# Kernel tuning notes

Measured on AMD Instinct MI355X. Metric: run time of the kernel, lower is better.

The kernel has to match this reference:

```python
import jax, jax.numpy as jnp
import numpy as np

B, L, D, U = 4, 1024, 256, 32

def setup_inputs() -> dict:
    key = jax.random.key(0)
    k1, k2, k3, k4 = jax.random.split(key, 4)
    return {
        "inputs": jax.random.normal(k1, (B, L, D), dtype=jnp.float32),
        "Wt": jax.random.normal(k2, (D, U), dtype=jnp.float32) * (1.0 / np.sqrt(D)),
        "Wx": jax.random.normal(k3, (D, U), dtype=jnp.float32) * (1.0 / np.sqrt(D)),
        "bh": jnp.zeros((U,), dtype=jnp.float32),
        "Wa": jax.random.normal(k4, (U, 1), dtype=jnp.float32) * (1.0 / np.sqrt(U)),
        "ba": jnp.zeros((1,), dtype=jnp.float32),
    }


def reference(inputs, Wt, Wx, bh, Wa, ba):
    # inputs: [B, L, D]
    q = jnp.einsum('bld,du->blu', inputs, Wt)  # [B, L, U]
    k = jnp.einsum('bld,du->blu', inputs, Wx)  # [B, L, U]
    # additive (Bahdanau) pairwise score: h is [B, L, L, U]
    h = jnp.tanh(q[:, :, None, :] + k[:, None, :, :] + bh)
    e = jnp.einsum('biju,u->bij', h, Wa[:, 0]) + ba[0]  # [B, L, L]
    a = jax.nn.softmax(e, axis=-1)  # stable softmax == exp(e-max)/sum
    v = jnp.einsum('bij,bjd->bid', a, inputs)  # weighted sum, [B, L, D]
    return v
```

## Files before the change

kernel.cpp:

```cpp
#include <hip/hip_runtime.h>
#include <hip/hip_bf16.h>
#include <math.h>

#define B_ 4
#define L_ 1024
#define D_ 256
#define U_ 32

#define SC2 2.8853900817779268f

#if __has_builtin(__builtin_amdgcn_exp2f)
#define EXP2(x) __builtin_amdgcn_exp2f(x)
#else
#define EXP2(x) exp2f(x)
#endif
#if __has_builtin(__builtin_amdgcn_rcpf)
#define RCP(x) __builtin_amdgcn_rcpf(x)
#else
#define RCP(x) (1.0f / (x))
#endif

typedef __attribute__((ext_vector_type(8))) short bf16x8;
typedef __attribute__((ext_vector_type(4))) float f32x4;
typedef unsigned long long u64;

__device__ __forceinline__ ushort f2bf(float f) {
  uint b = __float_as_uint(f);
  return (ushort)((b + 0x7fffu + ((b >> 16) & 1u)) >> 16);
}
__device__ __forceinline__ float bf2f(ushort u) {
  return __uint_as_float(((uint)u) << 16);
}
__device__ __forceinline__ uint packhl(float v) {
  ushort h = f2bf(v);
  ushort l = f2bf(v - bf2f(h));
  return (((uint)h) << 16) | (uint)l;
}
__device__ __forceinline__ u64 hi64(uint4 p) {
  return ((u64)(p.x >> 16)) | ((u64)(p.y >> 16) << 16) |
         ((u64)(p.z >> 16) << 32) | ((u64)(p.w >> 16) << 48);
}
__device__ __forceinline__ u64 lo64(uint4 p) {
  return ((u64)(p.x & 0xffffu)) | ((u64)(p.y & 0xffffu) << 16) |
         ((u64)(p.z & 0xffffu) << 32) | ((u64)(p.w & 0xffffu) << 48);
}

__global__ __launch_bounds__(256) void k_proj(
    const float* __restrict__ x, const float* __restrict__ Wt,
    const float* __restrict__ Wx, const float* __restrict__ bh,
    float* __restrict__ q2, float* __restrict__ k2, uint* __restrict__ xpk) {
  const int row = blockIdx.x;
  const int t = threadIdx.x;
  __shared__ float xr[D_];
  __shared__ float part[256];
  const float xv = x[(size_t)row * D_ + t];
  xr[t] = xv;
  {
    const int b = row >> 10;
    const int l = row & (L_ - 1);
    xpk[((size_t)b * D_ + t) * L_ + l] = packhl(xv);
  }
  __syncthreads();
  const int out = t & 63;
  const int u = out & 31;
  const int sel = out >> 5;
  const int p = t >> 6;
  const float* W = sel ? Wx : Wt;
  float s = 0.f;
  #pragma unroll
  for (int d = 0; d < 64; ++d) {
    const int dd = p * 64 + d;
    s = fmaf(xr[dd], W[dd * U_ + u], s);
  }
  part[t] = s;
  __syncthreads();
  if (t < 64) {
    const float v = part[t] + part[t + 64] + part[t + 128] + part[t + 192];
    if (sel == 0)
      q2[(size_t)row * U_ + u] = SC2 * (v + bh[u]);
    else
      k2[(size_t)row * U_ + u] = SC2 * v;
  }
}

__global__ __launch_bounds__(512) void k_scores(
    const float* __restrict__ q2, const float* __restrict__ k2,
    const float* __restrict__ Wa, uint* __restrict__ apk) {
  const int blk = blockIdx.x;
  const int b = blk >> 7;
  const int i0 = (blk & 127) * 8;
  const int t = threadIdx.x;
  __shared__ float e_lds[8][L_];

  const float* kb = k2 + (size_t)b * L_ * U_;
  float kr0[32], kr1[32];
  #pragma unroll
  for (int c = 0; c < 8; ++c) {
    const float4 v0 = *(const float4*)&kb[(size_t)t * U_ + 4 * c];
    const float4 v1 = *(const float4*)&kb[(size_t)(t + 512) * U_ + 4 * c];
    kr0[4 * c] = v0.x; kr0[4 * c + 1] = v0.y; kr0[4 * c + 2] = v0.z; kr0[4 * c + 3] = v0.w;
    kr1[4 * c] = v1.x; kr1[4 * c + 1] = v1.y; kr1[4 * c + 2] = v1.z; kr1[4 * c + 3] = v1.w;
  }

  float wa[32];
  float sumwa = 0.f;
  #pragma unroll
  for (int u = 0; u < 32; ++u) { wa[u] = Wa[u]; sumwa += wa[u]; }

  const float* qb = q2 + ((size_t)(b * L_ + i0)) * U_;
  #pragma unroll
  for (int i = 0; i < 8; ++i) {
    float qv[32];
    #pragma unroll
    for (int u = 0; u < 32; ++u) qv[u] = qb[i * U_ + u];
    float a00 = 0.f, a01 = 0.f, a10 = 0.f, a11 = 0.f;
    #pragma unroll
    for (int u = 0; u < 32; u += 2) {
      {
        const float y0 = qv[u] + kr0[u];
        const float r0 = RCP(EXP2(y0) + 1.f);
        a00 = fmaf(wa[u], r0, a00);
        const float y1 = qv[u] + kr1[u];
        const float r1 = RCP(EXP2(y1) + 1.f);
        a10 = fmaf(wa[u], r1, a10);
      }
      {
        const float y0 = qv[u + 1] + kr0[u + 1];
        const float r0 = RCP(EXP2(y0) + 1.f);
        a01 = fmaf(wa[u + 1], r0, a01);
        const float y1 = qv[u + 1] + kr1[u + 1];
        const float r1 = RCP(EXP2(y1) + 1.f);
        a11 = fmaf(wa[u + 1], r1, a11);
      }
    }
    e_lds[i][t]       = sumwa - 2.f * (a00 + a01);
    e_lds[i][t + 512] = sumwa - 2.f * (a10 + a11);
  }
  __syncthreads();

  const int w = t >> 6;
  const int lane = t & 63;
  float ev[16];
  float m = -1e30f;
  #pragma unroll
  for (int mm = 0; mm < 16; ++mm) {
    ev[mm] = e_lds[w][lane + 64 * mm];
    m = fmaxf(m, ev[mm]);
  }
  #pragma unroll
  for (int off = 32; off >= 1; off >>= 1) m = fmaxf(m, __shfl_xor(m, off, 64));
  float s = 0.f;
  #pragma unroll
  for (int mm = 0; mm < 16; ++mm) { ev[mm] = __expf(ev[mm] - m); s += ev[mm]; }
  #pragma unroll
  for (int off = 32; off >= 1; off >>= 1) s += __shfl_xor(s, off, 64);
  const float rinv = 1.0f / s;
  uint* arow = apk + ((size_t)(b * L_ + i0 + w)) * L_;
  #pragma unroll
  for (int mm = 0; mm < 16; ++mm) arow[lane + 64 * mm] = packhl(ev[mm] * rinv);
}

#define MFMA16(A, Bf, C) __builtin_amdgcn_mfma_f32_16x16x32_bf16(A, Bf, C, 0, 0, 0)

__global__ __launch_bounds__(256) void k_wsum(
    const uint* __restrict__ apk, const uint* __restrict__ xpk,
    float* __restrict__ out) {
  const int d0 = blockIdx.x * 64;
  const int i0 = blockIdx.y * 64;
  const int b  = blockIdx.z;
  const int t  = threadIdx.x;
  const int lane = t & 63;
  const int w  = t >> 6;
  const int wr = w >> 1;
  const int wc = w & 1;

  __shared__ f32x4 ldsv[4 * 64 * 8];
  char* const base = (char*)ldsv;

  const int r = t >> 2;
  const int q = t & 3;
  const uint* asrc = apk + ((size_t)(b * L_ + i0 + r)) * L_ + q * 16;
  const uint* xsrc = xpk + ((size_t)(b * D_ + d0 + r)) * L_ + q * 16;

  f32x4 acc00 = {0.f, 0.f, 0.f, 0.f}, acc01 = {0.f, 0.f, 0.f, 0.f};
  f32x4 acc10 = {0.f, 0.f, 0.f, 0.f}, acc11 = {0.f, 0.f, 0.f, 0.f};

  uint4 ra[4], rx[4];
  #pragma unroll
  for (int c = 0; c < 4; ++c) {
    ra[c] = *(const uint4*)(asrc + 4 * c);
    rx[c] = *(const uint4*)(xsrc + 4 * c);
  }

  for (int step = 0; step < 16; ++step) {
    __syncthreads();
    #pragma unroll
    for (int c = 0; c < 4; ++c) {
      const int jj = q * 16 + 4 * c;
      const int u = jj >> 3;
      const int half = (jj >> 2) & 1;
      const int off = r * 128 + ((u ^ (r & 7)) << 4) + half * 8;
      *(u64*)(base + off)          = hi64(ra[c]);
      *(u64*)(base + off + 8192)   = lo64(ra[c]);
      *(u64*)(base + off + 16384)  = hi64(rx[c]);
      *(u64*)(base + off + 24576)  = lo64(rx[c]);
    }
    if (step < 15) {
      #pragma unroll
      for (int c = 0; c < 4; ++c) {
        ra[c] = *(const uint4*)(asrc + (step + 1) * 64 + 4 * c);
        rx[c] = *(const uint4*)(xsrc + (step + 1) * 64 + 4 * c);
      }
    }
    __syncthreads();

    #pragma unroll
    for (int ks = 0; ks < 2; ++ks) {
      const int ub = ks * 4 + (lane >> 4);
      auto frag = [&](int plane, int rbase) -> bf16x8 {
        const int rr = rbase + (lane & 15);
        const int off = plane * 8192 + rr * 128 + ((ub ^ (rr & 7)) << 4);
        return *(const bf16x8*)(base + off);
      };
      const bf16x8 ah0 = frag(0, wr * 32), ah1 = frag(0, wr * 32 + 16);
      const bf16x8 al0 = frag(1, wr * 32), al1 = frag(1, wr * 32 + 16);
      const bf16x8 xh0 = frag(2, wc * 32), xh1 = frag(2, wc * 32 + 16);
      const bf16x8 xl0 = frag(3, wc * 32), xl1 = frag(3, wc * 32 + 16);
      acc00 = MFMA16(ah0, xh0, acc00); acc00 = MFMA16(al0, xh0, acc00); acc00 = MFMA16(ah0, xl0, acc00);
      acc01 = MFMA16(ah0, xh1, acc01); acc01 = MFMA16(al0, xh1, acc01); acc01 = MFMA16(ah0, xl1, acc01);
      acc10 = MFMA16(ah1, xh0, acc10); acc10 = MFMA16(al1, xh0, acc10); acc10 = MFMA16(ah1, xl0, acc10);
      acc11 = MFMA16(ah1, xh1, acc11); acc11 = MFMA16(al1, xh1, acc11); acc11 = MFMA16(ah1, xl1, acc11);
    }
  }

  const int crow = (lane >> 4) * 4;
  const int ccol = lane & 15;
  #pragma unroll
  for (int m2 = 0; m2 < 2; ++m2) {
    #pragma unroll
    for (int n2 = 0; n2 < 2; ++n2) {
      const f32x4 acc = m2 == 0 ? (n2 == 0 ? acc00 : acc01)
                                : (n2 == 0 ? acc10 : acc11);
      const int col = d0 + wc * 32 + n2 * 16 + ccol;
      #pragma unroll
      for (int jj = 0; jj < 4; ++jj) {
        const int rowi = i0 + wr * 32 + m2 * 16 + crow + jj;
        out[((size_t)(b * L_ + rowi)) * D_ + col] = acc[jj];
      }
    }
  }
}

extern "C" void kernel_launch(void* const* d_in, const int* in_sizes, int n_in,
                              void* d_out, int out_size, void* d_ws, size_t ws_size,
                              hipStream_t stream) {
  const float* x  = (const float*)d_in[0];
  const float* Wt = (const float*)d_in[1];
  const float* Wx = (const float*)d_in[2];
  const float* bh = (const float*)d_in[3];
  const float* Wa = (const float*)d_in[4];
  float* out = (float*)d_out;
  float* ws = (float*)d_ws;
  float* q2 = ws;
  float* k2 = ws + (size_t)B_ * L_ * U_;
  uint* apk = (uint*)(ws + (size_t)2 * B_ * L_ * U_);
  uint* xpk = apk + (size_t)B_ * L_ * L_;
  if (ws_size < (size_t)22020096) return;

  k_proj<<<B_ * L_, 256, 0, stream>>>(x, Wt, Wx, bh, q2, k2, xpk);
  k_scores<<<B_ * (L_ / 8), 512, 0, stream>>>(q2, k2, Wa, apk);
  dim3 g3(D_ / 64, L_ / 64, B_);
  k_wsum<<<g3, 256, 0, stream>>>(apk, xpk, out);
}
```

Baseline: 153.2 us.

## Split-K the weighted-sum GEMM, batch projection rows, and vectorize LDS stores

The weighted-sum kernel is split four ways along the key dimension, so the grid grows from 256 to 1024 blocks. Partial sums go to a workspace buffer and a new reduce kernel adds them. The projection kernel now handles 16 rows per block with float4 weight loads and writes coalesced uint4 packed-x stores instead of scattered scalar ones, and the wsum LDS staging uses 128-bit stores. The split adds a 16 MB partial-sum write and read plus an extra kernel launch.

Result: faster. 134.1 us, median of 2 (-12.5%).

```diff
diff --git a/kernel.cpp b/kernel.cpp
--- a/kernel.cpp
+++ b/kernel.cpp
@@ -6,6 +6,7 @@
 #define L_ 1024
 #define D_ 256
 #define U_ 32
+#define KSPLIT 4
 
 #define SC2 2.8853900817779268f
 
@@ -44,42 +45,75 @@
   return ((u64)(p.x & 0xffffu)) | ((u64)(p.y & 0xffffu) << 16) |
          ((u64)(p.z & 0xffffu) << 32) | ((u64)(p.w & 0xffffu) << 48);
 }
+__device__ __forceinline__ uint4 mk128(u64 lo, u64 hi) {
+  uint4 r;
+  r.x = (uint)lo; r.y = (uint)(lo >> 32);
+  r.z = (uint)hi; r.w = (uint)(hi >> 32);
+  return r;
+}
 
 __global__ __launch_bounds__(256) void k_proj(
     const float* __restrict__ x, const float* __restrict__ Wt,
     const float* __restrict__ Wx, const float* __restrict__ bh,
     float* __restrict__ q2, float* __restrict__ k2, uint* __restrict__ xpk) {
-  const int row = blockIdx.x;
+  const int blk = blockIdx.x;
+  const int b = blk >> 6;
+  const int l0 = (blk & 63) * 16;
   const int t = threadIdx.x;
-  __shared__ float xr[D_];
-  __shared__ float part[256];
-  const float xv = x[(size_t)row * D_ + t];
-  xr[t] = xv;
+  __shared__ float xr[16][D_];
+
+  const float* xbase = x + ((size_t)(b * L_ + l0)) * D_;
   {
-    const int b = row >> 10;
-    const int l = row & (L_ - 1);
-    xpk[((size_t)b * D_ + t) * L_ + l] = packhl(xv);
+    const int r = t >> 4;
+    const int c0 = (t & 15) * 16;
+    #pragma unroll
+    for (int c = 0; c < 4; ++c)
+      *(float4*)&xr[r][c0 + 4 * c] = *(const float4*)&xbase[(size_t)r * D_ + c0 + 4 * c];
   }
   __syncthreads();
-  const int out = t & 63;
-  const int u = out & 31;
-  const int sel = out >> 5;
-  const int p = t >> 6;
-  const float* W = sel ? Wx : Wt;
-  float s = 0.f;
-  #pragma unroll
-  for (int d = 0; d < 64; ++d) {
-    const int dd = p * 64 + d;
-    s = fmaf(xr[dd], W[dd * U_ + u], s);
-  }
-  part[t] = s;
-  __syncthreads();
-  if (t < 64) {
-    const float v = part[t] + part[t + 64] + part[t + 128] + part[t + 192];
-    if (sel == 0)
-      q2[(size_t)row * U_ + u] = SC2 * (v + bh[u]);
-    else
-      k2[(size_t)row * U_ + u] = SC2 * v;
+
+  {
+    const int rr = t >> 4;
+    const int g = t & 15;
+    const int sel = g >> 3;
+    const int u0 = (g & 7) * 4;
+    const float* W = sel ? Wx : Wt;
+    float acc0 = 0.f, acc1 = 0.f, acc2 = 0.f, acc3 = 0.f;
+    #pragma unroll 8
+    for (int d = 0; d < D_; ++d) {
+      const float4 w4 = *(const float4*)&W[d * U_ + u0];
+      const float xv = xr[rr][d];
+      acc0 = fmaf(xv, w4.x, acc0);
+      acc1 = fmaf(xv, w4.y, acc1);
+      acc2 = fmaf(xv, w4.z, acc2);
+      acc3 = fmaf(xv, w4.w, acc3);
+    }
+    const size_t orow = ((size_t)(b * L_ + l0 + rr)) * U_ + u0;
+    if (sel == 0) {
+      q2[orow]     = SC2 * (acc0 + bh[u0]);
+      q2[orow + 1] = SC2 * (acc1 + bh[u0 + 1]);
+      q2[orow + 2] = SC2 * (acc2 + bh[u0 + 2]);
+      q2[orow + 3] = SC2 * (acc3 + bh[u0 + 3]);
+    } else {
+      k2[orow]     = SC2 * acc0;
+      k2[orow + 1] = SC2 * acc1;
+      k2[orow + 2] = SC2 * acc2;
+      k2[orow + 3] = SC2 * acc3;
+    }
+  }
+
+  {
+    const int lq = t & 3;
+    #pragma unroll
+    for (int s = 0; s < 4; ++s) {
+      const int d = 64 * s + (t >> 2);
+      uint4 v;
+      v.x = packhl(xr[lq * 4 + 0][d]);
+      v.y = packhl(xr[lq * 4 + 1][d]);
+      v.z = packhl(xr[lq * 4 + 2][d]);
+      v.w = packhl(xr[lq * 4 + 3][d]);
+      *(uint4*)&xpk[((size_t)(b * D_ + d)) * L_ + l0 + lq * 4] = v;
+    }
   }
 }
 
@@ -164,10 +198,12 @@
 
 __global__ __launch_bounds__(256) void k_wsum(
     const uint* __restrict__ apk, const uint* __restrict__ xpk,
-    float* __restrict__ out) {
+    float* __restrict__ psum) {
   const int d0 = blockIdx.x * 64;
   const int i0 = blockIdx.y * 64;
-  const int b  = blockIdx.z;
+  const int bz = blockIdx.z;
+  const int b  = bz & 3;
+  const int ks0 = (bz >> 2) * 256;
   const int t  = threadIdx.x;
   const int lane = t & 63;
   const int w  = t >> 6;
@@ -177,10 +213,10 @@
   __shared__ f32x4 ldsv[4 * 64 * 8];
   char* const base = (char*)ldsv;
 
-  const int r = t >> 2;
-  const int q = t & 3;
-  const uint* asrc = apk + ((size_t)(b * L_ + i0 + r)) * L_ + q * 16;
-  const uint* xsrc = xpk + ((size_t)(b * D_ + d0 + r)) * L_ + q * 16;
+  const int r  = t >> 2;
+  const int kq = t & 3;
+  const uint* asrc = apk + ((size_t)(b * L_ + i0 + r)) * L_ + ks0 + kq * 16;
+  const uint* xsrc = xpk + ((size_t)(b * D_ + d0 + r)) * L_ + ks0 + kq * 16;
 
   f32x4 acc00 = {0.f, 0.f, 0.f, 0.f}, acc01 = {0.f, 0.f, 0.f, 0.f};
   f32x4 acc10 = {0.f, 0.f, 0.f, 0.f}, acc11 = {0.f, 0.f, 0.f, 0.f};
@@ -192,20 +228,18 @@
     rx[c] = *(const uint4*)(xsrc + 4 * c);
   }
 
-  for (int step = 0; step < 16; ++step) {
+  for (int step = 0; step < 4; ++step) {
     __syncthreads();
     #pragma unroll
-    for (int c = 0; c < 4; ++c) {
-      const int jj = q * 16 + 4 * c;
-      const int u = jj >> 3;
-      const int half = (jj >> 2) & 1;
-      const int off = r * 128 + ((u ^ (r & 7)) << 4) + half * 8;
-      *(u64*)(base + off)          = hi64(ra[c]);
-      *(u64*)(base + off + 8192)   = lo64(ra[c]);
-      *(u64*)(base + off + 16384)  = hi64(rx[c]);
-      *(u64*)(base + off + 24576)  = lo64(rx[c]);
-    }
-    if (step < 15) {
+    for (int h = 0; h < 2; ++h) {
+      const int ub = (kq * 2 + h) ^ (r & 7);
+      const int off = r * 128 + (ub << 4);
+      *(uint4*)(base + off)         = mk128(hi64(ra[2 * h]), hi64(ra[2 * h + 1]));
+      *(uint4*)(base + off + 8192)  = mk128(lo64(ra[2 * h]), lo64(ra[2 * h + 1]));
+      *(uint4*)(base + off + 16384) = mk128(hi64(rx[2 * h]), hi64(rx[2 * h + 1]));
+      *(uint4*)(base + off + 24576) = mk128(lo64(rx[2 * h]), lo64(rx[2 * h + 1]));
+    }
+    if (step < 3) {
       #pragma unroll
       for (int c = 0; c < 4; ++c) {
         ra[c] = *(const uint4*)(asrc + (step + 1) * 64 + 4 * c);
@@ -219,7 +253,7 @@
       const int ub = ks * 4 + (lane >> 4);
       auto frag = [&](int plane, int rbase) -> bf16x8 {
         const int rr = rbase + (lane & 15);
-        const int off = plane * 8192 + rr * 128 + ((ub ^ (rr & 7)) << 4);
+        const int off = plane * 8192 + rr * 128 + (((ub ^ (rr & 7))) << 4);
         return *(const bf16x8*)(base + off);
       };
       const bf16x8 ah0 = frag(0, wr * 32), ah1 = frag(0, wr * 32 + 16);
@@ -235,6 +269,7 @@
 
   const int crow = (lane >> 4) * 4;
   const int ccol = lane & 15;
+  float* pb = psum + (size_t)bz * L_ * D_;
   #pragma unroll
   for (int m2 = 0; m2 < 2; ++m2) {
     #pragma unroll
@@ -245,9 +280,28 @@
       #pragma unroll
       for (int jj = 0; jj < 4; ++jj) {
         const int rowi = i0 + wr * 32 + m2 * 16 + crow + jj;
-        out[((size_t)(b * L_ + rowi)) * D_ + col] = acc[jj];
+        pb[(size_t)rowi * D_ + col] = acc[jj];
       }
     }
+  }
+}
+
+__global__ __launch_bounds__(256) void k_reduce(
+    const float4* __restrict__ p, float4* __restrict__ o) {
+  const size_t n = (size_t)B_ * L_ * D_ / 4;
+  size_t i = (size_t)blockIdx.x * 256 + threadIdx.x;
+  const size_t stride = (size_t)gridDim.x * 256;
+  for (; i < n; i += stride) {
+    const float4 a = p[i];
+    const float4 b2 = p[i + n];
+    const float4 c = p[i + 2 * n];
+    const float4 d = p[i + 3 * n];
+    float4 r;
+    r.x = (a.x + b2.x) + (c.x + d.x);
+    r.y = (a.y + b2.y) + (c.y + d.y);
+    r.z = (a.z + b2.z) + (c.z + d.z);
+    r.w = (a.w + b2.w) + (c.w + d.w);
+    o[i] = r;
   }
 }
 
@@ -265,10 +319,12 @@
   float* k2 = ws + (size_t)B_ * L_ * U_;
   uint* apk = (uint*)(ws + (size_t)2 * B_ * L_ * U_);
   uint* xpk = apk + (size_t)B_ * L_ * L_;
-  if (ws_size < (size_t)22020096) return;
-
-  k_proj<<<B_ * L_, 256, 0, stream>>>(x, Wt, Wx, bh, q2, k2, xpk);
+  float* psum = (float*)(xpk + (size_t)B_ * D_ * L_);
+  if (ws_size < (size_t)38797312) return;
+
+  k_proj<<<B_ * L_ / 16, 256, 0, stream>>>(x, Wt, Wx, bh, q2, k2, xpk);
   k_scores<<<B_ * (L_ / 8), 512, 0, stream>>>(q2, k2, Wa, apk);
-  dim3 g3(D_ / 64, L_ / 64, B_);
-  k_wsum<<<g3, 256, 0, stream>>>(apk, xpk, out);
-}
+  dim3 g3(D_ / 64, L_ / 64, B_ * KSPLIT);
+  k_wsum<<<g3, 256, 0, stream>>>(apk, xpk, psum);
+  k_reduce<<<1024, 256, 0, stream>>>((const float4*)psum, (float4*)out);
+}
```
